# Performance work log

Hardware: AMD Instinct MI355X
Metric: run time of the kernel (lower is better)

The kernel has to match this reference:

```python
import jax, jax.numpy as jnp
import numpy as np

B, H, W = 2, 256, 256
N = B * H * W
E = 8 * N
CIN, CMID, COUT = 32, 64, 1
EPS = 1e-5
ELU_ALPHA = 0.1


def _elu(x):
    return jnp.where(x > 0, x, ELU_ALPHA * jnp.expm1(x))


def _bn(h, g, b, m, v):
    # inference-mode batchnorm over last (channel) axis
    return (h - m) * jax.lax.rsqrt(v + EPS) * g + b


def setup_inputs() -> dict:
    key = jax.random.key(0)
    ks = jax.random.split(key, 24)
    p = lambda k, s: jax.random.normal(k, s, jnp.float32) * 0.05
    return {
        "x": jax.random.normal(ks[0], (N, CIN), jnp.float32),
        "edge_index": jax.random.randint(ks[1], (2, E), 0, N),
        "edge_weight": jax.random.uniform(ks[2], (E, 2), jnp.float32),
        "batch": jnp.repeat(jnp.arange(B, dtype=jnp.int64), H * W),
        "nrows": H,
        "ncols": W,
        # Conv2d(in, mid, 3, padding=1, bias=False)
        "conv_w": p(ks[3], (CMID, CIN, 3, 3)),
        # BatchNorm2d(mid)
        "bn2_g": jnp.ones(CMID), "bn2_b": jnp.zeros(CMID),
        "bn2_m": p(ks[4], (CMID,)), "bn2_v": jnp.abs(p(ks[5], (CMID,))) + 1.0,
        # GCNConv(mid, mid, improved=True)
        "gcn_w": p(ks[6], (CMID, CMID)), "gcn_b": p(ks[7], (CMID,)),
        # BatchNorm(mid) -- same module reused twice in the Sequential
        "bn1_g": jnp.ones(CMID), "bn1_b": jnp.zeros(CMID),
        "bn1_m": p(ks[8], (CMID,)), "bn1_v": jnp.abs(p(ks[9], (CMID,))) + 1.0,
        # TransformerConv(mid, mid, heads=1, edge_dim=2)
        "wq": p(ks[10], (CMID, CMID)), "bq": p(ks[11], (CMID,)),
        "wk": p(ks[12], (CMID, CMID)), "bk": p(ks[13], (CMID,)),
        "wv": p(ks[14], (CMID, CMID)), "bv": p(ks[15], (CMID,)),
        "we": p(ks[16], (CMID, 2)),                      # lin_edge, bias=False
        "wskip": p(ks[17], (CMID, CMID)), "bskip": p(ks[18], (CMID,)),
        # final Linear(mid, out)
        "wl": p(ks[19], (COUT, CMID)), "bl": p(ks[20], (COUT,)),
    }


def reference(x, edge_index, edge_weight, batch, nrows, ncols,
              conv_w, bn2_g, bn2_b, bn2_m, bn2_v,
              gcn_w, gcn_b, bn1_g, bn1_b, bn1_m, bn1_v,
              wq, bq, wk, bk, wv, bv, we, wskip, bskip, wl, bl):
    nbatch = B  # batch.unique().size(0)
    # GraphToConv: (N, C) -> (B, C, H, W)
    img = x.reshape(nbatch, nrows, ncols, CIN).transpose(0, 3, 1, 2)
    h = jax.lax.conv_general_dilated(img, conv_w, (1, 1), "SAME",
                                     dimension_numbers=("NCHW", "OIHW", "NCHW"))
    h = _bn(h, bn2_g[:, None, None], bn2_b[:, None, None],
            bn2_m[:, None, None], bn2_v[:, None, None])
    h = _elu(h)  # dropout2d is identity in eval
    # ConvToGraph: (B, C, H, W) -> (N, C)
    h = h.transpose(0, 2, 3, 1).reshape(N, CMID)

    # GCNConv(improved=True): A_hat = A + 2I
    row, col = edge_index[0], edge_index[1]
    ew = edge_weight[:, 1]
    si = jnp.arange(N)
    row2 = jnp.concatenate([row, si])
    col2 = jnp.concatenate([col, si])
    w2 = jnp.concatenate([ew, jnp.full((N,), 2.0, h.dtype)])
    deg = jax.ops.segment_sum(w2, col2, N)
    dinv = jnp.where(deg > 0, jax.lax.rsqrt(deg), 0.0)
    norm = dinv[row2] * w2 * dinv[col2]  # [E+N]
    hw = h @ gcn_w.T
    h = jax.ops.segment_sum(norm[:, None] * hw[row2], col2, N) + gcn_b
    h = _elu(_bn(h, bn1_g, bn1_b, bn1_m, bn1_v))

    # TransformerConv(heads=1, edge_dim=2)
    q = h @ wq.T + bq
    k = h @ wk.T + bk
    v = h @ wv.T + bv
    e = edge_weight @ we.T  # [E, CMID]
    ke = k[row] + e
    alpha = jnp.sum(q[col] * ke, axis=-1) / np.sqrt(CMID).astype(np.float32)
    amax = jax.ops.segment_max(alpha, col, N)
    amax = jnp.where(jnp.isfinite(amax), amax, 0.0)
    ex = jnp.exp(alpha - amax[col])
    denom = jax.ops.segment_sum(ex, col, N)
    attn = ex / denom[col]  # softmax over incoming edges
    msg = (v[row] + e) * attn[:, None]
    out = jax.ops.segment_sum(msg, col, N) + (h @ wskip.T + bskip)  # root_weight
    out = _bn(out, bn1_g, bn1_b, bn1_m, bn1_v)
    return out @ wl.T + bl
```

## Files before the change

### kernel.cpp

```cpp
#include <hip/hip_runtime.h>
#include <hip/hip_fp16.h>
#include <math.h>

#define CIN   32
#define CMID  64
#define HH    256
#define WW    256
#define EPSBN 1e-5f
#define ELU_A 0.1f
#define LOG2E_DIV8 0.18033688f

typedef _Float16 half8 __attribute__((ext_vector_type(8)));
typedef _Float16 half2v __attribute__((ext_vector_type(2)));
typedef float    floatx4 __attribute__((ext_vector_type(4)));

#if __has_builtin(__builtin_amdgcn_fdot2)
#define DOT2(a, b, c) __builtin_amdgcn_fdot2((a), (b), (c), false)
#else
#define DOT2(a, b, c) ((c) + (float)(a)[0] * (float)(b)[0] + (float)(a)[1] * (float)(b)[1])
#endif

__device__ __forceinline__ float elu_f(float x) {
    return x > 0.f ? x : ELU_A * (__expf(x) - 1.f);
}
__device__ __forceinline__ float wave_sum64(float v) {
#pragma unroll
    for (int off = 32; off > 0; off >>= 1) v += __shfl_xor(v, off, 64);
    return v;
}
__device__ __forceinline__ half2v shfl_xor_h2(half2v v, int off) {
    int b = __builtin_bit_cast(int, v);
    b = __shfl_xor(b, off, 64);
    return __builtin_bit_cast(half2v, b);
}

__global__ void prep_all(const float* __restrict__ cw,
                         const float* __restrict__ g2, const float* __restrict__ b2,
                         const float* __restrict__ m2, const float* __restrict__ v2,
                         const float* __restrict__ w_gcn, const float* __restrict__ w_q,
                         const float* __restrict__ w_skip, const float* __restrict__ w_k,
                         const float* __restrict__ w_v,
                         const float* __restrict__ g1, const float* __restrict__ b1,
                         const float* __restrict__ m1, const float* __restrict__ v1,
                         const float* __restrict__ wl, const float* __restrict__ bl,
                         const float* __restrict__ we,
                         __half* __restrict__ wt16, float* __restrict__ ebias,
                         __half* __restrict__ wlin, float* __restrict__ wls,
                         float* __restrict__ consts, int* __restrict__ cnt, int N) {
    int idx = blockIdx.x * 256 + threadIdx.x;
    if (idx < N) cnt[idx] = 0;
    if (idx < 5 * 2 * 4 * 64 * 8) {
        int j = idx & 7, lane = (idx >> 3) & 63, rest = idx >> 9;
        int ot = rest & 3, kt = (rest >> 2) & 1, mat = rest >> 3;
        int o = ot * 16 + (lane & 15);
        int k = kt * 32 + (lane >> 4) * 8 + j;
        const float* W = (mat == 0) ? w_gcn : (mat == 1) ? w_q :
                         (mat == 2) ? w_skip : (mat == 3) ? w_k : w_v;
        wlin[idx] = __float2half(W[o * 64 + k]);
    }
    if (idx < 36 * 64 * 8) {
        int j = idx & 7, lane = (idx >> 3) & 63, to = idx >> 9;
        int tap = to >> 2, otile = to & 3;
        int o = otile * 16 + (lane & 15);
        int k = (lane >> 4) * 8 + j;
        float s = g2[o] * rsqrtf(v2[o] + EPSBN);
        wt16[idx] = __float2half(cw[(o * 32 + k) * 9 + tap] * s);
    }
    if (idx < 64) {
        float s = g2[idx] * rsqrtf(v2[idx] + EPSBN);
        ebias[idx] = b2[idx] - m2[idx] * s;
    }
    if (blockIdx.x == 0 && threadIdx.x < 64) {
        int c = threadIdx.x;
        float s = g1[c] * rsqrtf(v1[c] + EPSBN);
        float w = wl[c] * s;
        wls[c] = w;
        float p0 = w * we[2 * c];
        float p1 = w * we[2 * c + 1];
        float p2 = wl[c] * (b1[c] - m1[c] * s);
        p0 = wave_sum64(p0);
        p1 = wave_sum64(p1);
        p2 = wave_sum64(p2);
        if (c == 0) { consts[0] = p0; consts[1] = p1; consts[2] = p2 + bl[0]; }
    }
}

__global__ __launch_bounds__(256, 2) void conv_mfma(
        const float* __restrict__ x, const __half* __restrict__ wt16,
        const float* __restrict__ ebias, const float* __restrict__ dinv,
        __half* __restrict__ h0, int ngroups) {
    const int lane = threadIdx.x & 63;
    const int wid  = (blockIdx.x * 256 + threadIdx.x) >> 6;
    const int n16 = lane & 15, quad = lane >> 4;

    half8 bf[36];
#pragma unroll
    for (int t = 0; t < 36; ++t)
        bf[t] = *reinterpret_cast<const half8*>(wt16 + ((size_t)t * 64 + lane) * 8);
    float eb[4];
#pragma unroll
    for (int ot = 0; ot < 4; ++ot) eb[ot] = ebias[ot * 16 + n16];

    for (int gidx = wid * 4; gidx < wid * 4 + 4; ++gidx) {
        if (gidx >= ngroups) return;
        const int br = gidx >> 4;
        const int c0 = (gidx & 15) << 4;
        const int r  = br & (HH - 1);
        floatx4 acc[4] = {{0.f,0.f,0.f,0.f},{0.f,0.f,0.f,0.f},
                          {0.f,0.f,0.f,0.f},{0.f,0.f,0.f,0.f}};
#pragma unroll
        for (int dr = -1; dr <= 1; ++dr) {
            int rr = r + dr;
            if (rr < 0 || rr >= HH) continue;
            const float* xrow = x + (size_t)(br + dr) * WW * CIN;
#pragma unroll
            for (int dc = -1; dc <= 1; ++dc) {
                int cc = c0 + n16 + dc;
                half8 a = {};
                if (cc >= 0 && cc < WW) {
                    const float* xp = xrow + cc * CIN + quad * 8;
                    float4 f0 = *reinterpret_cast<const float4*>(xp);
                    float4 f1 = *reinterpret_cast<const float4*>(xp + 4);
                    a[0] = (_Float16)f0.x; a[1] = (_Float16)f0.y;
                    a[2] = (_Float16)f0.z; a[3] = (_Float16)f0.w;
                    a[4] = (_Float16)f1.x; a[5] = (_Float16)f1.y;
                    a[6] = (_Float16)f1.z; a[7] = (_Float16)f1.w;
                }
                const int tap = (dr + 1) * 3 + (dc + 1);
#pragma unroll
                for (int ot = 0; ot < 4; ++ot)
                    acc[ot] = __builtin_amdgcn_mfma_f32_16x16x32_f16(a, bf[tap * 4 + ot], acc[ot], 0, 0, 0);
            }
        }
        const int nbase = br * WW + c0;
        float dv[4];
#pragma unroll
        for (int reg = 0; reg < 4; ++reg) dv[reg] = dinv[nbase + quad * 4 + reg];
        __half* hp = h0 + (size_t)nbase * 64;
#pragma unroll
        for (int ot = 0; ot < 4; ++ot) {
#pragma unroll
            for (int reg = 0; reg < 4; ++reg) {
                int px = quad * 4 + reg;
                float val = elu_f(acc[ot][reg] + eb[ot]) * dv[reg];
                hp[(size_t)px * 64 + ot * 16 + n16] = __float2half(val);
            }
        }
    }
}

__global__ void hist_kernel(const int* __restrict__ col, int* __restrict__ cnt,
                            unsigned short* __restrict__ rank, int E) {
    int e = blockIdx.x * 256 + threadIdx.x;
    if (e < E) rank[e] = (unsigned short)atomicAdd(&cnt[col[e]], 1);
}

__global__ void scan1(const int* __restrict__ cnt, int* __restrict__ bsum) {
    __shared__ int s[256];
    int t = threadIdx.x;
    int4 c = reinterpret_cast<const int4*>(cnt)[blockIdx.x * 256 + t];
    s[t] = c.x + c.y + c.z + c.w;
    __syncthreads();
    for (int off = 128; off > 0; off >>= 1) {
        if (t < off) s[t] += s[t + off];
        __syncthreads();
    }
    if (t == 0) bsum[blockIdx.x] = s[0];
}

__global__ void scan2(const int* __restrict__ bsum, int* __restrict__ boff, int nb) {
    int t = threadIdx.x;
    int b0 = (t < nb) ? bsum[t] : 0;
    int b1 = (t + 64 < nb) ? bsum[t + 64] : 0;
    int v0 = b0, v1 = b1;
#pragma unroll
    for (int off = 1; off < 64; off <<= 1) {
        int u0 = __shfl_up(v0, off, 64);
        int u1 = __shfl_up(v1, off, 64);
        if (t >= off) { v0 += u0; v1 += u1; }
    }
    int tot0 = __shfl(v0, 63, 64);
    if (t < nb) boff[t] = v0 - b0;
    if (t + 64 < nb) boff[t + 64] = tot0 + v1 - b1;
}

__global__ void scan3(const int* __restrict__ cnt, const int* __restrict__ boff,
                      int* __restrict__ rowptr, int Ntot) {
    __shared__ int lds[256];
    int t = threadIdx.x;
    int4 c = reinterpret_cast<const int4*>(cnt)[blockIdx.x * 256 + t];
    int s1 = c.x, s2 = s1 + c.y, s3 = s2 + c.z, s4 = s3 + c.w;
    lds[t] = s4;
    __syncthreads();
    for (int off = 1; off < 256; off <<= 1) {
        int v = (t >= off) ? lds[t - off] : 0;
        __syncthreads();
        lds[t] += v;
        __syncthreads();
    }
    int excl = (t > 0 ? lds[t - 1] : 0) + boff[blockIdx.x];
    int base = (blockIdx.x * 256 + t) * 4;
    rowptr[base + 0] = excl;
    rowptr[base + 1] = excl + s1;
    rowptr[base + 2] = excl + s2;
    rowptr[base + 3] = excl + s3;
    if (base + 4 == Ntot) rowptr[Ntot] = excl + s4;
}

__global__ void scatter_kernel(const int* __restrict__ ei, const float* __restrict__ ew,
                               const unsigned short* __restrict__ rank,
                               const int* __restrict__ rowptr,
                               int2* __restrict__ edges, int E) {
    int e = blockIdx.x * 256 + threadIdx.x;
    if (e >= E) return;
    int c = ei[E + e];
    int pos = rowptr[c] + (int)rank[e];
    if (pos < 0 || pos >= E) return;
    __half2 hw = __floats2half2_rn(ew[2 * e], ew[2 * e + 1]);
    int2 pk;
    pk.x = ei[e];
    pk.y = *reinterpret_cast<int*>(&hw);
    edges[pos] = pk;
}

__global__ void deg_kernel(const int* __restrict__ rowptr, const int2* __restrict__ edges,
                           float* __restrict__ dinv, int2* __restrict__ rowpair, int Ntot) {
    int n = blockIdx.x * 256 + threadIdx.x;
    if (n >= Ntot) return;
    int p0 = rowptr[n], p1 = rowptr[n + 1];
    rowpair[n] = make_int2(p0, p1);
    float s = 2.f;
    for (int p = p0; p < p1; ++p) {
        int wbits = edges[p].y;
        s += __high2float(*reinterpret_cast<__half2*>(&wbits));
    }
    dinv[n] = rsqrtf(s);
}

__global__ __launch_bounds__(256) void gcn_gather(
        const __half* __restrict__ h0s, const int2* __restrict__ edges,
        const int2* __restrict__ rowpair,
        const float* __restrict__ dinv, __half* __restrict__ agg16, int Ntot) {
    const int lane = threadIdx.x & 63;
    const int grp = lane >> 3, t = lane & 7;
    const int n = blockIdx.x * 4 + (threadIdx.x >> 6);
    if (n >= Ntot) return;
    const float din = dinv[n];
    const int2 rp = rowpair[n];
    const int p0 = rp.x, p1 = rp.y;

    half2v acc2[4] = {};
    if (grp == 0) {
        half8 hs = *reinterpret_cast<const half8*>(h0s + (size_t)n * 64 + 8 * t);
        const half2v* h2 = reinterpret_cast<const half2v*>(&hs);
        _Float16 c = (_Float16)(2.f * din);
        half2v ch = {c, c};
#pragma unroll
        for (int i = 0; i < 4; ++i) acc2[i] = ch * h2[i];
    }
    for (int p = p0; p < p1; p += 16) {
        int pe0 = p + grp, pe1 = p + 8 + grp;
        bool a0 = pe0 < p1, a1 = pe1 < p1;
        int2 e0 = edges[a0 ? pe0 : p0];
        int2 e1 = edges[a1 ? pe1 : p0];
        float w0 = __high2float(*reinterpret_cast<__half2*>(&e0.y));
        float w1 = __high2float(*reinterpret_cast<__half2*>(&e1.y));
        float c0 = a0 ? w0 * din : 0.f;
        float c1 = a1 ? w1 * din : 0.f;
        half8 hv0 = *reinterpret_cast<const half8*>(h0s + (size_t)e0.x * 64 + 8 * t);
        half8 hv1 = *reinterpret_cast<const half8*>(h0s + (size_t)e1.x * 64 + 8 * t);
        const half2v* h20 = reinterpret_cast<const half2v*>(&hv0);
        const half2v* h21 = reinterpret_cast<const half2v*>(&hv1);
        _Float16 c0h = (_Float16)c0, c1h = (_Float16)c1;
        half2v ch0 = {c0h, c0h}, ch1 = {c1h, c1h};
#pragma unroll
        for (int i = 0; i < 4; ++i) {
            acc2[i] += ch0 * h20[i];
            acc2[i] += ch1 * h21[i];
        }
    }
#pragma unroll
    for (int off = 8; off <= 32; off <<= 1)
#pragma unroll
        for (int i = 0; i < 4; ++i)
            acc2[i] += shfl_xor_h2(acc2[i], off);
    if (grp == 0) {
        half8 ov;
#pragma unroll
        for (int i = 0; i < 4; ++i) { ov[2 * i] = acc2[i][0]; ov[2 * i + 1] = acc2[i][1]; }
        *reinterpret_cast<half8*>(agg16 + (size_t)n * 64 + 8 * t) = ov;
    }
}

#define LDS_STRIDE 72
__global__ __launch_bounds__(256) void mfma_fused(
        const __half* __restrict__ in16, const __half* __restrict__ wb,
        const float* __restrict__ gcn_b, const float* __restrict__ g,
        const float* __restrict__ b, const float* __restrict__ m,
        const float* __restrict__ v,
        const float* __restrict__ bq, const float* __restrict__ bs,
        const float* __restrict__ bk, const float* __restrict__ bv,
        const float* __restrict__ wls, const float* __restrict__ we,
        __half* __restrict__ qout, __half* __restrict__ kout,
        float* __restrict__ vdot, float4* __restrict__ aux, int ngroups) {
    __shared__ _Float16 lds_h1[4][16 * LDS_STRIDE];
    const int lane = threadIdx.x & 63;
    const int n16 = lane & 15, quad = lane >> 4;
    const int wv_ = threadIdx.x >> 6;
    _Float16* myld = lds_h1[wv_];

    half8 bf1[2][4];
#pragma unroll
    for (int kt = 0; kt < 2; ++kt)
#pragma unroll
        for (int ot = 0; ot < 4; ++ot)
            bf1[kt][ot] = *reinterpret_cast<const half8*>(wb + (((size_t)kt * 4 + ot) * 64 + lane) * 8);
    half8 bf2[4][2][4];
#pragma unroll
    for (int mt = 0; mt < 4; ++mt)
#pragma unroll
        for (int kt = 0; kt < 2; ++kt)
#pragma unroll
            for (int ot = 0; ot < 4; ++ot)
                bf2[mt][kt][ot] = *reinterpret_cast<const half8*>(
                    wb + ((((size_t)(mt + 1) * 2 + kt) * 4 + ot) * 64 + lane) * 8);

    float scl[4], shf[4], bbq[4], bbs[4], bbk[4], bbv[4], wlsv[4], we0v[4], we1v[4];
#pragma unroll
    for (int ot = 0; ot < 4; ++ot) {
        int o = ot * 16 + n16;
        float s = g[o] * rsqrtf(v[o] + EPSBN);
        scl[ot] = s;
        shf[ot] = (gcn_b[o] - m[o]) * s + b[o];
        bbq[ot] = bq[o]; bbs[ot] = bs[o]; bbk[ot] = bk[o]; bbv[ot] = bv[o];
        wlsv[ot] = wls[o];
        we0v[ot] = we[2 * o]; we1v[ot] = we[2 * o + 1];
    }

    const int wid    = blockIdx.x * 4 + wv_;
    const int stride = gridDim.x * 4;
    const int trips  = (ngroups + stride - 1) / stride;
    for (int it = 0; it < trips; ++it) {
        const int gi = wid + it * stride;
        const bool active = gi < ngroups;
        const int nbase = gi * 16;
        if (active) {
            half8 a0 = *reinterpret_cast<const half8*>(in16 + (size_t)(nbase + n16) * 64 + quad * 8);
            half8 a1 = *reinterpret_cast<const half8*>(in16 + (size_t)(nbase + n16) * 64 + 32 + quad * 8);
            floatx4 acc[4] = {{0,0,0,0},{0,0,0,0},{0,0,0,0},{0,0,0,0}};
#pragma unroll
            for (int ot = 0; ot < 4; ++ot) {
                acc[ot] = __builtin_amdgcn_mfma_f32_16x16x32_f16(a0, bf1[0][ot], acc[ot], 0, 0, 0);
                acc[ot] = __builtin_amdgcn_mfma_f32_16x16x32_f16(a1, bf1[1][ot], acc[ot], 0, 0, 0);
            }
#pragma unroll
            for (int ot = 0; ot < 4; ++ot)
#pragma unroll
                for (int reg = 0; reg < 4; ++reg) {
                    float val = elu_f(acc[ot][reg] * scl[ot] + shf[ot]);
                    myld[(quad * 4 + reg) * LDS_STRIDE + ot * 16 + n16] = (_Float16)val;
                }
        }
        __syncthreads();
        if (active) {
            half8 c0 = *reinterpret_cast<const half8*>(&myld[n16 * LDS_STRIDE + quad * 8]);
            half8 c1 = *reinterpret_cast<const half8*>(&myld[n16 * LDS_STRIDE + 32 + quad * 8]);
            floatx4 aq[4] = {{0,0,0,0},{0,0,0,0},{0,0,0,0},{0,0,0,0}};
            floatx4 as[4] = {{0,0,0,0},{0,0,0,0},{0,0,0,0},{0,0,0,0}};
            floatx4 ak[4] = {{0,0,0,0},{0,0,0,0},{0,0,0,0},{0,0,0,0}};
            floatx4 av[4] = {{0,0,0,0},{0,0,0,0},{0,0,0,0},{0,0,0,0}};
#pragma unroll
            for (int ot = 0; ot < 4; ++ot) {
                aq[ot] = __builtin_amdgcn_mfma_f32_16x16x32_f16(c0, bf2[0][0][ot], aq[ot], 0, 0, 0);
                aq[ot] = __builtin_amdgcn_mfma_f32_16x16x32_f16(c1, bf2[0][1][ot], aq[ot], 0, 0, 0);
                as[ot] = __builtin_amdgcn_mfma_f32_16x16x32_f16(c0, bf2[1][0][ot], as[ot], 0, 0, 0);
                as[ot] = __builtin_amdgcn_mfma_f32_16x16x32_f16(c1, bf2[1][1][ot], as[ot], 0, 0, 0);
                ak[ot] = __builtin_amdgcn_mfma_f32_16x16x32_f16(c0, bf2[2][0][ot], ak[ot], 0, 0, 0);
                ak[ot] = __builtin_amdgcn_mfma_f32_16x16x32_f16(c1, bf2[2][1][ot], ak[ot], 0, 0, 0);
                av[ot] = __builtin_amdgcn_mfma_f32_16x16x32_f16(c0, bf2[3][0][ot], av[ot], 0, 0, 0);
                av[ot] = __builtin_amdgcn_mfma_f32_16x16x32_f16(c1, bf2[3][1][ot], av[ot], 0, 0, 0);
            }
            float psd[4] = {0,0,0,0}, pq0[4] = {0,0,0,0}, pq1[4] = {0,0,0,0}, pvd[4] = {0,0,0,0};
#pragma unroll
            for (int ot = 0; ot < 4; ++ot)
#pragma unroll
                for (int reg = 0; reg < 4; ++reg) {
                    int px = nbase + quad * 4 + reg;
                    size_t off64 = (size_t)px * 64 + ot * 16 + n16;
                    float qv = aq[ot][reg] + bbq[ot];
                    qout[off64] = __float2half(qv);
                    kout[off64] = __float2half(ak[ot][reg] + bbk[ot]);
                    psd[reg] = fmaf(wlsv[ot], as[ot][reg] + bbs[ot], psd[reg]);
                    pvd[reg] = fmaf(wlsv[ot], av[ot][reg] + bbv[ot], pvd[reg]);
                    pq0[reg] = fmaf(we0v[ot], qv, pq0[reg]);
                    pq1[reg] = fmaf(we1v[ot], qv, pq1[reg]);
                }
#pragma unroll
            for (int off = 1; off <= 8; off <<= 1)
#pragma unroll
                for (int reg = 0; reg < 4; ++reg) {
                    psd[reg] += __shfl_xor(psd[reg], off, 64);
                    pvd[reg] += __shfl_xor(pvd[reg], off, 64);
                    pq0[reg] += __shfl_xor(pq0[reg], off, 64);
                    pq1[reg] += __shfl_xor(pq1[reg], off, 64);
                }
            if (n16 == 0) {
#pragma unroll
                for (int reg = 0; reg < 4; ++reg) {
                    aux[nbase + quad * 4 + reg] =
                        make_float4(pq0[reg], pq1[reg], psd[reg], 0.f);
                    vdot[nbase + quad * 4 + reg] = pvd[reg];
                }
            }
        }
        __syncthreads();
    }
}

__global__ __launch_bounds__(256) void attn_out(
        const __half* __restrict__ qh, const __half* __restrict__ kout,
        const float* __restrict__ vdot, const float4* __restrict__ aux,
        const int2* __restrict__ edges, const int2* __restrict__ rowpair,
        const float* __restrict__ consts, float* __restrict__ out, int Ntot) {
    const int lane = threadIdx.x & 63;
    const int grp = lane >> 3, t = lane & 7;
    const int n = blockIdx.x * 4 + (threadIdx.x >> 6);
    if (n >= Ntot) return;

    half8 q8 = *reinterpret_cast<const half8*>(qh + (size_t)n * 64 + 8 * t);
    const half2v* q2 = reinterpret_cast<const half2v*>(&q8);
    float4 ax = aux[n];
    const float qe0s = ax.x * LOG2E_DIV8, qe1s = ax.y * LOG2E_DIV8;
    const float c0 = consts[0], c1 = consts[1], c2 = consts[2];
    const int2 rp = rowpair[n];
    const int p0 = rp.x, p1 = rp.y;

    float l = 0.f, sx = 0.f, sy = 0.f, pd = 0.f;
    for (int p = p0; p < p1; p += 16) {
        int pe0 = p + grp, pe1 = p + 8 + grp;
        bool a0 = pe0 < p1, a1 = pe1 < p1;
        int2 e0 = edges[a0 ? pe0 : p0];
        int2 e1 = edges[a1 ? pe1 : p0];
        float2 w0 = __half22float2(*reinterpret_cast<__half2*>(&e0.y));
        float2 w1 = __half22float2(*reinterpret_cast<__half2*>(&e1.y));
        half8 k80 = *reinterpret_cast<const half8*>(kout + (size_t)e0.x * 64 + 8 * t);
        half8 k81 = *reinterpret_cast<const half8*>(kout + (size_t)e1.x * 64 + 8 * t);
        float vd0 = vdot[e0.x];
        float vd1 = vdot[e1.x];
        const half2v* k20 = reinterpret_cast<const half2v*>(&k80);
        const half2v* k21 = reinterpret_cast<const half2v*>(&k81);
        float prod0 = 0.f, prod1 = 0.f;
#pragma unroll
        for (int i = 0; i < 4; ++i) {
            prod0 = DOT2(q2[i], k20[i], prod0);
            prod1 = DOT2(q2[i], k21[i], prod1);
        }
#pragma unroll
        for (int off = 1; off <= 4; off <<= 1) {
            prod0 += __shfl_xor(prod0, off, 64);
            prod1 += __shfl_xor(prod1, off, 64);
        }
        float ex0 = a0 ? exp2f(fmaf(qe1s, w0.y, fmaf(qe0s, w0.x, prod0 * LOG2E_DIV8))) : 0.f;
        float ex1 = a1 ? exp2f(fmaf(qe1s, w1.y, fmaf(qe0s, w1.x, prod1 * LOG2E_DIV8))) : 0.f;
        l += ex0 + ex1;
        sx = fmaf(ex0, w0.x, sx); sx = fmaf(ex1, w1.x, sx);
        sy = fmaf(ex0, w0.y, sy); sy = fmaf(ex1, w1.y, sy);
        pd = fmaf(ex0, vd0, pd);  pd = fmaf(ex1, vd1, pd);
    }
    float u = pd + fmaf(sx, c0, sy * c1);
#pragma unroll
    for (int off = 8; off <= 32; off <<= 1) {
        l += __shfl_xor(l, off, 64);
        u += __shfl_xor(u, off, 64);
    }
    if (lane == 0) {
        float inv_l = (l > 0.f) ? 1.f / l : 0.f;
        out[n] = inv_l * u + ax.z + c2;
    }
}

extern "C" void kernel_launch(void* const* d_in, const int* in_sizes, int n_in,
                              void* d_out, int out_size, void* d_ws, size_t ws_size,
                              hipStream_t stream) {
    const float* x      = (const float*)d_in[0];
    const int*   ei     = (const int*)d_in[1];
    const float* ew     = (const float*)d_in[2];
    const float* conv_w = (const float*)d_in[6];
    const float* bn2_g  = (const float*)d_in[7];
    const float* bn2_b  = (const float*)d_in[8];
    const float* bn2_m  = (const float*)d_in[9];
    const float* bn2_v  = (const float*)d_in[10];
    const float* gcn_w  = (const float*)d_in[11];
    const float* gcn_b  = (const float*)d_in[12];
    const float* bn1_g  = (const float*)d_in[13];
    const float* bn1_b  = (const float*)d_in[14];
    const float* bn1_m  = (const float*)d_in[15];
    const float* bn1_v  = (const float*)d_in[16];
    const float* wq     = (const float*)d_in[17];
    const float* bq     = (const float*)d_in[18];
    const float* wk     = (const float*)d_in[19];
    const float* bk     = (const float*)d_in[20];
    const float* wv     = (const float*)d_in[21];
    const float* bv     = (const float*)d_in[22];
    const float* we     = (const float*)d_in[23];
    const float* wskip  = (const float*)d_in[24];
    const float* bskip  = (const float*)d_in[25];
    const float* wl     = (const float*)d_in[26];
    const float* bl     = (const float*)d_in[27];

    const int N = in_sizes[0] / CIN;
    const int E = in_sizes[1] / 2;

    char* p = (char*)d_ws;
    auto alloc = [&](size_t bytes) {
        void* r = (void*)p;
        p += (bytes + 255) & ~(size_t)255;
        return r;
    };
    __half* wt16    = (__half*)alloc(36 * 64 * 8 * 2);
    float*  ebias   = (float*)alloc(64 * 4);
    __half* wlin    = (__half*)alloc(5 * 2 * 4 * 64 * 8 * 2);
    float*  wls     = (float*)alloc(64 * 4);
    float*  consts  = (float*)alloc(64 * 4);
    __half* bufA    = (__half*)alloc((size_t)N * 64 * 2);
    __half* kout    = (__half*)alloc((size_t)N * 64 * 2);
    __half* bufQ    = (__half*)alloc((size_t)N * 64 * 2);
    __half* agg16   = (__half*)alloc((size_t)N * 64 * 2);
    float*  vdot    = (float*)alloc((size_t)N * 4);
    float4* aux     = (float4*)alloc((size_t)N * 16);
    float*  dinv    = (float*)alloc((size_t)N * 4);
    int*    cnt     = (int*)alloc((size_t)N * 4);
    unsigned short* rank = (unsigned short*)alloc((size_t)E * 2);
    int*    rowptr  = (int*)alloc((size_t)(N + 1) * 4);
    int2*   rowpair = (int2*)alloc((size_t)N * 8);
    int2*   edges   = (int2*)alloc((size_t)E * 8);
    int*    bsum    = (int*)alloc(256 * 4);
    int*    boff    = (int*)alloc(256 * 4);

    prep_all<<<(N + 255) / 256, 256, 0, stream>>>(
        conv_w, bn2_g, bn2_b, bn2_m, bn2_v,
        gcn_w, wq, wskip, wk, wv,
        bn1_g, bn1_b, bn1_m, bn1_v, wl, bl, we,
        wt16, ebias, wlin, wls, consts, cnt, N);

    hist_kernel<<<(E + 255) / 256, 256, 0, stream>>>(ei + E, cnt, rank, E);
    scan1<<<N / 1024, 256, 0, stream>>>(cnt, bsum);
    scan2<<<1, 64, 0, stream>>>(bsum, boff, N / 1024);
    scan3<<<N / 1024, 256, 0, stream>>>(cnt, boff, rowptr, N);
    scatter_kernel<<<(E + 255) / 256, 256, 0, stream>>>(ei, ew, rank, rowptr, edges, E);
    deg_kernel<<<(N + 255) / 256, 256, 0, stream>>>(rowptr, edges, dinv, rowpair, N);

    const int ngroups = N / 16;
    conv_mfma<<<ngroups / 16, 256, 0, stream>>>(x, wt16, ebias, dinv, bufA, ngroups);

    gcn_gather<<<(N + 3) / 4, 256, 0, stream>>>(bufA, edges, rowpair, dinv, agg16, N);

    mfma_fused<<<512, 256, 0, stream>>>(agg16, wlin, gcn_b,
                                        bn1_g, bn1_b, bn1_m, bn1_v,
                                        bq, bskip, bk, bv, wls, we,
                                        bufQ, kout, vdot, aux, ngroups);

    attn_out<<<(N + 3) / 4, 256, 0, stream>>>(bufQ, kout, vdot, aux, edges, rowpair,
                                              consts, (float*)d_out, N);
}
```

Measured before the change: 319.7 us.

## Replace global-atomic CSR build with two-level bucketed counting sort

Builds the destination-sorted edge list with a two-pass bucket sort: per-block LDS histograms over 64-node buckets, a bucket scan, a scatter into bucket order, and a per-bucket finalize that sorts by node in LDS and computes row ranges and inverse degree. This replaces per-edge global atomics on node counters, three scan kernels, a scatter and a serial degree loop. The aim is to cut global atomic contention and random memory traffic. In exchange it adds staging and intermediate buffers plus an extra pass over the edges. It also caps buckets at MAXB edges, which silently truncates denser buckets, and it packs the row index into 24 bits.

```diff
diff --git a/kernel.cpp b/kernel.cpp
--- a/kernel.cpp
+++ b/kernel.cpp
@@ -9,6 +9,10 @@
 #define EPSBN 1e-5f
 #define ELU_A 0.1f
 #define LOG2E_DIV8 0.18033688f
+
+#define NBUCK 2048
+#define EPB   4096
+#define MAXB  2048
 
 typedef _Float16 half8 __attribute__((ext_vector_type(8)));
 typedef _Float16 half2v __attribute__((ext_vector_type(2)));
@@ -46,9 +50,8 @@
                          const float* __restrict__ we,
                          __half* __restrict__ wt16, float* __restrict__ ebias,
                          __half* __restrict__ wlin, float* __restrict__ wls,
-                         float* __restrict__ consts, int* __restrict__ cnt, int N) {
+                         float* __restrict__ consts) {
     int idx = blockIdx.x * 256 + threadIdx.x;
-    if (idx < N) cnt[idx] = 0;
     if (idx < 5 * 2 * 4 * 64 * 8) {
         int j = idx & 7, lane = (idx >> 3) & 63, rest = idx >> 9;
         int ot = rest & 3, kt = (rest >> 2) & 1, mat = rest >> 3;
@@ -149,92 +152,153 @@
     }
 }
 
-__global__ void hist_kernel(const int* __restrict__ col, int* __restrict__ cnt,
-                            unsigned short* __restrict__ rank, int E) {
-    int e = blockIdx.x * 256 + threadIdx.x;
-    if (e < E) rank[e] = (unsigned short)atomicAdd(&cnt[col[e]], 1);
-}
-
-__global__ void scan1(const int* __restrict__ cnt, int* __restrict__ bsum) {
-    __shared__ int s[256];
-    int t = threadIdx.x;
-    int4 c = reinterpret_cast<const int4*>(cnt)[blockIdx.x * 256 + t];
-    s[t] = c.x + c.y + c.z + c.w;
+__global__ __launch_bounds__(256) void bucket_hist(
+        const int* __restrict__ ei, const float* __restrict__ ew,
+        int2* __restrict__ staging, unsigned short* __restrict__ lrank,
+        int* __restrict__ priv, int E) {
+    __shared__ int hist[NBUCK];
+    const int t = threadIdx.x, blk = blockIdx.x;
+#pragma unroll
+    for (int i = t; i < NBUCK; i += 256) hist[i] = 0;
     __syncthreads();
-    for (int off = 128; off > 0; off >>= 1) {
-        if (t < off) s[t] += s[t + off];
-        __syncthreads();
-    }
-    if (t == 0) bsum[blockIdx.x] = s[0];
-}
-
-__global__ void scan2(const int* __restrict__ bsum, int* __restrict__ boff, int nb) {
-    int t = threadIdx.x;
-    int b0 = (t < nb) ? bsum[t] : 0;
-    int b1 = (t + 64 < nb) ? bsum[t + 64] : 0;
-    int v0 = b0, v1 = b1;
+    const int base = blk * EPB;
+#pragma unroll 4
+    for (int j = 0; j < EPB / 256; ++j) {
+        int e = base + j * 256 + t;
+        if (e >= E) break;
+        int col = ei[E + e];
+        int row = ei[e];
+        float2 w = reinterpret_cast<const float2*>(ew)[e];
+        int b = col >> 6;
+        int lr = atomicAdd(&hist[b], 1);
+        __half2 hw = __floats2half2_rn(w.x, w.y);
+        int2 pk;
+        pk.x = row | ((col & 63) << 24);
+        pk.y = *reinterpret_cast<int*>(&hw);
+        staging[e] = pk;
+        lrank[e] = (unsigned short)lr;
+    }
+    __syncthreads();
+#pragma unroll
+    for (int i = t; i < NBUCK; i += 256) priv[blk * NBUCK + i] = hist[i];
+}
+
+__global__ void bscan1(int* __restrict__ priv, int* __restrict__ btot, int nblk) {
+    const int b = blockIdx.x * 4 + (threadIdx.x >> 6);
+    const int l = threadIdx.x & 63;
+    const int per = nblk / 64;
+    int v[8];
+    int s = 0;
+#pragma unroll 4
+    for (int j = 0; j < per; ++j) { v[j] = priv[(l * per + j) * NBUCK + b]; s += v[j]; }
+    int inc = s;
 #pragma unroll
     for (int off = 1; off < 64; off <<= 1) {
-        int u0 = __shfl_up(v0, off, 64);
-        int u1 = __shfl_up(v1, off, 64);
-        if (t >= off) { v0 += u0; v1 += u1; }
-    }
-    int tot0 = __shfl(v0, 63, 64);
-    if (t < nb) boff[t] = v0 - b0;
-    if (t + 64 < nb) boff[t + 64] = tot0 + v1 - b1;
-}
-
-__global__ void scan3(const int* __restrict__ cnt, const int* __restrict__ boff,
-                      int* __restrict__ rowptr, int Ntot) {
+        int u = __shfl_up(inc, off, 64);
+        if (l >= off) inc += u;
+    }
+    int excl = inc - s;
+#pragma unroll 4
+    for (int j = 0; j < per; ++j) {
+        int c = v[j];
+        priv[(l * per + j) * NBUCK + b] = excl;
+        excl += c;
+    }
+    if (l == 63) btot[b] = inc;
+}
+
+__global__ void bscan2(const int* __restrict__ btot, int* __restrict__ bbase) {
     __shared__ int lds[256];
-    int t = threadIdx.x;
-    int4 c = reinterpret_cast<const int4*>(cnt)[blockIdx.x * 256 + t];
-    int s1 = c.x, s2 = s1 + c.y, s3 = s2 + c.z, s4 = s3 + c.w;
-    lds[t] = s4;
+    const int t = threadIdx.x;
+    int v[8];
+    int s = 0;
+#pragma unroll
+    for (int j = 0; j < 8; ++j) { v[j] = btot[t * 8 + j]; s += v[j]; }
+    lds[t] = s;
     __syncthreads();
     for (int off = 1; off < 256; off <<= 1) {
-        int v = (t >= off) ? lds[t - off] : 0;
+        int u = (t >= off) ? lds[t - off] : 0;
         __syncthreads();
-        lds[t] += v;
+        lds[t] += u;
         __syncthreads();
     }
-    int excl = (t > 0 ? lds[t - 1] : 0) + boff[blockIdx.x];
-    int base = (blockIdx.x * 256 + t) * 4;
-    rowptr[base + 0] = excl;
-    rowptr[base + 1] = excl + s1;
-    rowptr[base + 2] = excl + s2;
-    rowptr[base + 3] = excl + s3;
-    if (base + 4 == Ntot) rowptr[Ntot] = excl + s4;
-}
-
-__global__ void scatter_kernel(const int* __restrict__ ei, const float* __restrict__ ew,
-                               const unsigned short* __restrict__ rank,
-                               const int* __restrict__ rowptr,
-                               int2* __restrict__ edges, int E) {
-    int e = blockIdx.x * 256 + threadIdx.x;
-    if (e >= E) return;
-    int c = ei[E + e];
-    int pos = rowptr[c] + (int)rank[e];
-    if (pos < 0 || pos >= E) return;
-    __half2 hw = __floats2half2_rn(ew[2 * e], ew[2 * e + 1]);
-    int2 pk;
-    pk.x = ei[e];
-    pk.y = *reinterpret_cast<int*>(&hw);
-    edges[pos] = pk;
-}
-
-__global__ void deg_kernel(const int* __restrict__ rowptr, const int2* __restrict__ edges,
-                           float* __restrict__ dinv, int2* __restrict__ rowpair, int Ntot) {
-    int n = blockIdx.x * 256 + threadIdx.x;
-    if (n >= Ntot) return;
-    int p0 = rowptr[n], p1 = rowptr[n + 1];
-    rowpair[n] = make_int2(p0, p1);
-    float s = 2.f;
-    for (int p = p0; p < p1; ++p) {
-        int wbits = edges[p].y;
-        s += __high2float(*reinterpret_cast<__half2*>(&wbits));
-    }
-    dinv[n] = rsqrtf(s);
+    int excl = (t > 0) ? lds[t - 1] : 0;
+#pragma unroll
+    for (int j = 0; j < 8; ++j) { bbase[t * 8 + j] = excl; excl += v[j]; }
+    if (t == 255) bbase[NBUCK] = excl;
+}
+
+__global__ __launch_bounds__(256) void bucket_scatter(
+        const int* __restrict__ ei, const int2* __restrict__ staging,
+        const unsigned short* __restrict__ lrank, const int* __restrict__ priv,
+        const int* __restrict__ bbase, int2* __restrict__ emid, int E) {
+    const int i = blockIdx.x * 256 + threadIdx.x;
+    if (i * 4 >= E) return;
+    int4 col4 = reinterpret_cast<const int4*>(ei + E)[i];
+    ushort4 rk = reinterpret_cast<const ushort4*>(lrank)[i];
+    const int blk = (i * 4) >> 12;
+    int b0 = col4.x >> 6, b1 = col4.y >> 6, b2 = col4.z >> 6, b3 = col4.w >> 6;
+    int p0 = bbase[b0] + priv[blk * NBUCK + b0] + (int)rk.x;
+    int p1 = bbase[b1] + priv[blk * NBUCK + b1] + (int)rk.y;
+    int p2 = bbase[b2] + priv[blk * NBUCK + b2] + (int)rk.z;
+    int p3 = bbase[b3] + priv[blk * NBUCK + b3] + (int)rk.w;
+    int2 s0 = staging[i * 4 + 0];
+    int2 s1 = staging[i * 4 + 1];
+    int2 s2 = staging[i * 4 + 2];
+    int2 s3 = staging[i * 4 + 3];
+    if (p0 >= 0 && p0 < E) emid[p0] = s0;
+    if (p1 >= 0 && p1 < E) emid[p1] = s1;
+    if (p2 >= 0 && p2 < E) emid[p2] = s2;
+    if (p3 >= 0 && p3 < E) emid[p3] = s3;
+}
+
+__global__ __launch_bounds__(256) void bucket_finalize(
+        const int2* __restrict__ emid, const int* __restrict__ bbase,
+        int2* __restrict__ edges, int2* __restrict__ rowpair,
+        float* __restrict__ dinv, int Ntot) {
+    __shared__ int ncnt[64];
+    __shared__ float nws[64];
+    __shared__ unsigned short lrk[MAXB];
+    const int b = blockIdx.x, t = threadIdx.x;
+    const int start = bbase[b], end = bbase[b + 1];
+    const int sz = min(end - start, MAXB);
+    if (t < 64) { ncnt[t] = 0; nws[t] = 0.f; }
+    __syncthreads();
+    for (int s = t; s < sz; s += 256) {
+        int2 r = emid[start + s];
+        int node = (r.x >> 24) & 63;
+        int lr = atomicAdd(&ncnt[node], 1);
+        lrk[s] = (unsigned short)lr;
+        float w1 = __high2float(*reinterpret_cast<__half2*>(&r.y));
+        atomicAdd(&nws[node], w1);
+    }
+    __syncthreads();
+    if (t < 64) {
+        int c = ncnt[t];
+        int inc = c;
+#pragma unroll
+        for (int off = 1; off < 64; off <<= 1) {
+            int u = __shfl_up(inc, off, 64);
+            if (t >= off) inc += u;
+        }
+        int excl = inc - c;
+        ncnt[t] = excl;
+        int node = b * 64 + t;
+        if (node < Ntot) {
+            rowpair[node] = make_int2(start + excl, start + excl + c);
+            dinv[node] = rsqrtf(2.f + nws[t]);
+        }
+    }
+    __syncthreads();
+    for (int s = t; s < sz; s += 256) {
+        int2 r = emid[start + s];
+        int node = (r.x >> 24) & 63;
+        int pos = start + ncnt[node] + (int)lrk[s];
+        int2 o;
+        o.x = r.x & 0x00FFFFFF;
+        o.y = r.y;
+        edges[pos] = o;
+    }
 }
 
 __global__ __launch_bounds__(256) void gcn_gather(
@@ -529,26 +593,27 @@
     float*  vdot    = (float*)alloc((size_t)N * 4);
     float4* aux     = (float4*)alloc((size_t)N * 16);
     float*  dinv    = (float*)alloc((size_t)N * 4);
-    int*    cnt     = (int*)alloc((size_t)N * 4);
-    unsigned short* rank = (unsigned short*)alloc((size_t)E * 2);
-    int*    rowptr  = (int*)alloc((size_t)(N + 1) * 4);
     int2*   rowpair = (int2*)alloc((size_t)N * 8);
     int2*   edges   = (int2*)alloc((size_t)E * 8);
-    int*    bsum    = (int*)alloc(256 * 4);
-    int*    boff    = (int*)alloc(256 * 4);
-
-    prep_all<<<(N + 255) / 256, 256, 0, stream>>>(
+    int2*   staging = (int2*)alloc((size_t)E * 8);
+    int2*   emid    = (int2*)alloc((size_t)E * 8);
+    unsigned short* lrank = (unsigned short*)alloc((size_t)E * 2);
+    int*    priv    = (int*)alloc((size_t)(E / EPB) * NBUCK * 4);
+    int*    btot    = (int*)alloc((size_t)NBUCK * 4);
+    int*    bbase   = (int*)alloc((size_t)(NBUCK + 1) * 4);
+
+    prep_all<<<80, 256, 0, stream>>>(
         conv_w, bn2_g, bn2_b, bn2_m, bn2_v,
         gcn_w, wq, wskip, wk, wv,
         bn1_g, bn1_b, bn1_m, bn1_v, wl, bl, we,
-        wt16, ebias, wlin, wls, consts, cnt, N);
-
-    hist_kernel<<<(E + 255) / 256, 256, 0, stream>>>(ei + E, cnt, rank, E);
-    scan1<<<N / 1024, 256, 0, stream>>>(cnt, bsum);
-    scan2<<<1, 64, 0, stream>>>(bsum, boff, N / 1024);
-    scan3<<<N / 1024, 256, 0, stream>>>(cnt, boff, rowptr, N);
-    scatter_kernel<<<(E + 255) / 256, 256, 0, stream>>>(ei, ew, rank, rowptr, edges, E);
-    deg_kernel<<<(N + 255) / 256, 256, 0, stream>>>(rowptr, edges, dinv, rowpair, N);
+        wt16, ebias, wlin, wls, consts);
+
+    const int nblkA = E / EPB;
+    bucket_hist<<<nblkA, 256, 0, stream>>>(ei, ew, staging, lrank, priv, E);
+    bscan1<<<NBUCK / 4, 256, 0, stream>>>(priv, btot, nblkA);
+    bscan2<<<1, 256, 0, stream>>>(btot, bbase);
+    bucket_scatter<<<E / 1024, 256, 0, stream>>>(ei, staging, lrank, priv, bbase, emid, E);
+    bucket_finalize<<<NBUCK, 256, 0, stream>>>(emid, bbase, edges, rowpair, dinv, N);
 
     const int ngroups = N / 16;
     conv_mfma<<<ngroups / 16, 256, 0, stream>>>(x, wt16, ebias, dinv, bufA, ngroups);
```

After: 294.2 us. 8.0% less time.
